# Kernel optimization log

Measured on AMD Instinct MI355X. Metric: run time of the kernel, lower is better.

The kernel has to match this reference:

```python
import jax, jax.numpy as jnp
import numpy as np

B, S, D = 4, 4096, 1024

def setup_inputs() -> dict:
    key = jax.random.key(0)
    k1, k2, k3 = jax.random.split(key, 3)
    x = jax.random.normal(k1, (B, S, D), dtype=jnp.float32)
    # learned scalar decay logit; original initializes to 0.9 then sigmoids it
    decay_param = jnp.float32(0.9)
    # gate weight [D, D]; original inits to zeros (identity module) -- use small
    # random values so the baseline exercises the full math path
    W_gate = jax.random.normal(k3, (D, D), dtype=jnp.float32) * 0.02
    return {"x": x, "decay_param": decay_param, "W_gate": W_gate}

def reference(x, decay_param, W_gate):
    # x: [B, S, D]
    d = jax.nn.sigmoid(decay_param)  # scalar

    def step(state, x_t):
        # state, x_t: [B, D]
        new = d * state + (1.0 - d) * x_t
        return new, new

    x_t_first = jnp.swapaxes(x, 0, 1)  # [S, B, D]
    init = jnp.zeros((x.shape[0], x.shape[2]), dtype=x.dtype)
    _, causal = jax.lax.scan(step, init, x_t_first)  # [S, B, D]
    causal = jnp.swapaxes(causal, 0, 1)  # [B, S, D]
    # nn.Linear(D, D, bias=False): y = causal @ W^T
    return x + jnp.einsum('bsd,ed->bse', causal, W_gate)
```

## Files before the change

### kernel.cpp

```cpp
#include <hip/hip_runtime.h>
#include <hip/hip_bf16.h>

#define B_DIM 4
#define S_DIM 4096
#define D_DIM 1024
#define M_TOT (B_DIM * S_DIM)
#define LOOKBACK 64
#define CHUNK 128
#define NT (D_DIM / 64)

typedef unsigned short us;
typedef __attribute__((ext_vector_type(8))) short bf16x8;
typedef __attribute__((ext_vector_type(4))) float f32x4;
typedef __attribute__((ext_vector_type(4))) unsigned short u16x4;

__device__ __forceinline__ us f2bf(float f) {
  unsigned int u = __builtin_bit_cast(unsigned int, f);
  u += 0x7fffu + ((u >> 16) & 1u);
  return (us)(u >> 16);
}

__global__ __launch_bounds__(256) void scan_kernel(
    const float* __restrict__ x, const float* __restrict__ dp,
    us* __restrict__ causal) {
  const float dcy = 1.0f / (1.0f + expf(-dp[0]));
  const float omd = 1.0f - dcy;
  const int d0 = blockIdx.x * 512 + threadIdx.x;
  const int s0 = blockIdx.y * CHUNK;
  const size_t base = (size_t)blockIdx.z * S_DIM * D_DIM + d0;
  float st0 = 0.f, st1 = 0.f;
  if (s0 > 0) {
    const float* px = x + base + (size_t)(s0 - LOOKBACK) * D_DIM;
#pragma unroll 8
    for (int i = 0; i < LOOKBACK; ++i) {
      st0 = dcy * st0 + omd * px[0];
      st1 = dcy * st1 + omd * px[256];
      px += D_DIM;
    }
  }
  const float* px = x + base + (size_t)s0 * D_DIM;
  us* pc = causal + base + (size_t)s0 * D_DIM;
#pragma unroll 8
  for (int i = 0; i < CHUNK; ++i) {
    st0 = dcy * st0 + omd * px[0];
    st1 = dcy * st1 + omd * px[256];
    pc[0]   = f2bf(st0);
    pc[256] = f2bf(st1);
    px += D_DIM;
    pc += D_DIM;
  }
}

__global__ __launch_bounds__(256) void convw_kernel(
    const float* __restrict__ W, us* __restrict__ Wb) {
  const int i = (blockIdx.x * 256 + threadIdx.x) * 4;
  const float4 v = *(const float4*)(W + i);
  u16x4 o;
  o.x = f2bf(v.x); o.y = f2bf(v.y); o.z = f2bf(v.z); o.w = f2bf(v.w);
  *(u16x4*)(Wb + i) = o;
}

__global__ __launch_bounds__(256) void gemm_kernel(
    const us* __restrict__ A,
    const us* __restrict__ Bw,
    const float* __restrict__ x,
    float* __restrict__ out) {
  __shared__ us As[128 * 64];
  __shared__ us Bs[128 * 64];

  const int bid = blockIdx.x;
  const int swz = (bid & 7) * 128 + (bid >> 3);
  const int m0 = (swz >> 3) * 128;
  const int n0 = (swz & 7) * 128;

  const int tid = threadIdx.x;
  const int lane = tid & 63;
  const int wave = tid >> 6;
  const int wr = wave >> 1;
  const int wc = wave & 1;
  const int lrow = lane & 15;
  const int ls   = lane >> 4;
  const int koff0 = ((0 + ls) ^ (lane & 7)) * 8;
  const int koff1 = ((4 + ls) ^ (lane & 7)) * 8;
  const int arow = (wr * 64 + lrow) * 64;
  const int brow = (wc * 64 + lrow) * 64;

  f32x4 acc[4][4];
#pragma unroll
  for (int i = 0; i < 4; ++i)
#pragma unroll
    for (int j = 0; j < 4; ++j) acc[i][j] = (f32x4)0.f;

  for (int t = 0; t < NT; ++t) {
    const int k0 = t * 64;
#pragma unroll
    for (int it = 0; it < 4; ++it) {
      const int c = it * 256 + tid;
      const int r = c >> 3;
      const int c16 = (c & 7) ^ (r & 7);
      __builtin_amdgcn_global_load_lds(
          (const __attribute__((address_space(1))) void*)(A +
              (size_t)(m0 + r) * D_DIM + k0 + c16 * 8),
          (__attribute__((address_space(3))) void*)(As + c * 8), 16, 0, 0);
      __builtin_amdgcn_global_load_lds(
          (const __attribute__((address_space(1))) void*)(Bw +
              (size_t)(n0 + r) * D_DIM + k0 + c16 * 8),
          (__attribute__((address_space(3))) void*)(Bs + c * 8), 16, 0, 0);
    }
    __syncthreads();

    bf16x8 a[4][2], b[4][2];
#pragma unroll
    for (int mi = 0; mi < 4; ++mi) {
      a[mi][0] = *(const bf16x8*)(As + arow + mi * 16 * 64 + koff0);
      a[mi][1] = *(const bf16x8*)(As + arow + mi * 16 * 64 + koff1);
    }
#pragma unroll
    for (int nj = 0; nj < 4; ++nj) {
      b[nj][0] = *(const bf16x8*)(Bs + brow + nj * 16 * 64 + koff0);
      b[nj][1] = *(const bf16x8*)(Bs + brow + nj * 16 * 64 + koff1);
    }
#pragma unroll
    for (int ks = 0; ks < 2; ++ks)
#pragma unroll
      for (int mi = 0; mi < 4; ++mi)
#pragma unroll
        for (int nj = 0; nj < 4; ++nj)
          acc[mi][nj] = __builtin_amdgcn_mfma_f32_16x16x32_bf16(
              a[mi][ks], b[nj][ks], acc[mi][nj], 0, 0, 0);
    __syncthreads();
  }

#pragma unroll
  for (int mi = 0; mi < 4; ++mi)
#pragma unroll
    for (int nj = 0; nj < 4; ++nj) {
      const int ocol = n0 + wc * 64 + nj * 16 + lrow;
      const int orow0 = m0 + wr * 64 + mi * 16 + ls * 4;
#pragma unroll
      for (int r = 0; r < 4; ++r) {
        const size_t idx = (size_t)(orow0 + r) * D_DIM + ocol;
        out[idx] = x[idx] + acc[mi][nj][r];
      }
    }
}

extern "C" void kernel_launch(void* const* d_in, const int* in_sizes, int n_in,
                              void* d_out, int out_size, void* d_ws, size_t ws_size,
                              hipStream_t stream) {
  const float* x  = (const float*)d_in[0];
  const float* dp = (const float*)d_in[1];
  const float* W  = (const float*)d_in[2];
  float* out = (float*)d_out;

  us* causal = (us*)d_ws;
  us* Wb = (us*)((char*)d_ws + (size_t)M_TOT * D_DIM * 2);

  dim3 g_scan(D_DIM / 512, S_DIM / CHUNK, B_DIM);
  scan_kernel<<<g_scan, 256, 0, stream>>>(x, dp, causal);

  convw_kernel<<<(D_DIM * D_DIM) / (256 * 4), 256, 0, stream>>>(W, Wb);

  gemm_kernel<<<(M_TOT / 128) * (D_DIM / 128), 256, 0, stream>>>(
      causal, Wb, x, out);
}
```

Measured before the change: 80.39 us.

## Double-buffer LDS in GEMM, shrink N tile to 64, remap block swizzle

The GEMM now double-buffers its A and B shared-memory tiles, issuing the async global-to-LDS loads for the next K step while the current step's MFMAs run, with one barrier per iteration. The output tile shrinks from 128x128 to 128x64, which doubles the grid, and the block-index swizzle is remapped. A launch-bounds occupancy hint of 3 blocks per CU is added. The intent is to hide global load latency and raise occupancy, at the cost of less operand reuse per block and more total A-tile traffic.

```diff
diff --git a/kernel.cpp b/kernel.cpp
--- a/kernel.cpp
+++ b/kernel.cpp
@@ -60,18 +60,18 @@
   *(u16x4*)(Wb + i) = o;
 }
 
-__global__ __launch_bounds__(256) void gemm_kernel(
+__global__ __launch_bounds__(256, 3) void gemm_kernel(
     const us* __restrict__ A,
     const us* __restrict__ Bw,
     const float* __restrict__ x,
     float* __restrict__ out) {
-  __shared__ us As[128 * 64];
-  __shared__ us Bs[128 * 64];
+  __shared__ us As[2][128 * 64];
+  __shared__ us Bs[2][64 * 64];
 
   const int bid = blockIdx.x;
-  const int swz = (bid & 7) * 128 + (bid >> 3);
-  const int m0 = (swz >> 3) * 128;
-  const int n0 = (swz & 7) * 128;
+  const int q = bid >> 3;
+  const int m0 = (((bid & 7) << 4) + (q >> 4)) * 128;
+  const int n0 = (q & 15) * 64;
 
   const int tid = threadIdx.x;
   const int lane = tid & 63;
@@ -83,59 +83,72 @@
   const int koff0 = ((0 + ls) ^ (lane & 7)) * 8;
   const int koff1 = ((4 + ls) ^ (lane & 7)) * 8;
   const int arow = (wr * 64 + lrow) * 64;
-  const int brow = (wc * 64 + lrow) * 64;
+  const int brow = (wc * 32 + lrow) * 64;
 
-  f32x4 acc[4][4];
+  f32x4 acc[4][2];
 #pragma unroll
   for (int i = 0; i < 4; ++i)
 #pragma unroll
-    for (int j = 0; j < 4; ++j) acc[i][j] = (f32x4)0.f;
+    for (int j = 0; j < 2; ++j) acc[i][j] = (f32x4)0.f;
+
+#define STAGE(t, p)                                                            \
+  {                                                                            \
+    _Pragma("unroll")                                                          \
+    for (int it = 0; it < 4; ++it) {                                           \
+      const int c = it * 256 + tid;                                            \
+      const int r = c >> 3;                                                    \
+      const int slot = (c & 7) ^ (r & 7);                                      \
+      __builtin_amdgcn_global_load_lds(                                        \
+          (const __attribute__((address_space(1))) void*)(A +                  \
+              (size_t)(m0 + r) * D_DIM + (t) * 64 + slot * 8),                 \
+          (__attribute__((address_space(3))) void*)(&As[p][0] + c * 8),        \
+          16, 0, 0);                                                           \
+    }                                                                          \
+    _Pragma("unroll")                                                          \
+    for (int it = 0; it < 2; ++it) {                                           \
+      const int c = it * 256 + tid;                                            \
+      const int r = c >> 3;                                                    \
+      const int slot = (c & 7) ^ (r & 7);                                      \
+      __builtin_amdgcn_global_load_lds(                                        \
+          (const __attribute__((address_space(1))) void*)(Bw +                 \
+              (size_t)(n0 + r) * D_DIM + (t) * 64 + slot * 8),                 \
+          (__attribute__((address_space(3))) void*)(&Bs[p][0] + c * 8),        \
+          16, 0, 0);                                                           \
+    }                                                                          \
+  }
+
+  STAGE(0, 0);
+  __syncthreads();
 
   for (int t = 0; t < NT; ++t) {
-    const int k0 = t * 64;
+    const int p = t & 1;
+    if (t + 1 < NT) STAGE(t + 1, p ^ 1);
+
 #pragma unroll
-    for (int it = 0; it < 4; ++it) {
-      const int c = it * 256 + tid;
-      const int r = c >> 3;
-      const int c16 = (c & 7) ^ (r & 7);
-      __builtin_amdgcn_global_load_lds(
-          (const __attribute__((address_space(1))) void*)(A +
-              (size_t)(m0 + r) * D_DIM + k0 + c16 * 8),
-          (__attribute__((address_space(3))) void*)(As + c * 8), 16, 0, 0);
-      __builtin_amdgcn_global_load_lds(
-          (const __attribute__((address_space(1))) void*)(Bw +
-              (size_t)(n0 + r) * D_DIM + k0 + c16 * 8),
-          (__attribute__((address_space(3))) void*)(Bs + c * 8), 16, 0, 0);
-    }
-    __syncthreads();
-
-    bf16x8 a[4][2], b[4][2];
+    for (int ks = 0; ks < 2; ++ks) {
+      const int koff = ks ? koff1 : koff0;
+      bf16x8 a[4], b[2];
 #pragma unroll
-    for (int mi = 0; mi < 4; ++mi) {
-      a[mi][0] = *(const bf16x8*)(As + arow + mi * 16 * 64 + koff0);
-      a[mi][1] = *(const bf16x8*)(As + arow + mi * 16 * 64 + koff1);
-    }
+      for (int mi = 0; mi < 4; ++mi)
+        a[mi] = *(const bf16x8*)(&As[p][0] + arow + mi * 1024 + koff);
 #pragma unroll
-    for (int nj = 0; nj < 4; ++nj) {
-      b[nj][0] = *(const bf16x8*)(Bs + brow + nj * 16 * 64 + koff0);
-      b[nj][1] = *(const bf16x8*)(Bs + brow + nj * 16 * 64 + koff1);
-    }
-#pragma unroll
-    for (int ks = 0; ks < 2; ++ks)
+      for (int nj = 0; nj < 2; ++nj)
+        b[nj] = *(const bf16x8*)(&Bs[p][0] + brow + nj * 1024 + koff);
 #pragma unroll
       for (int mi = 0; mi < 4; ++mi)
 #pragma unroll
-        for (int nj = 0; nj < 4; ++nj)
+        for (int nj = 0; nj < 2; ++nj)
           acc[mi][nj] = __builtin_amdgcn_mfma_f32_16x16x32_bf16(
-              a[mi][ks], b[nj][ks], acc[mi][nj], 0, 0, 0);
+              a[mi], b[nj], acc[mi][nj], 0, 0, 0);
+    }
     __syncthreads();
   }
 
 #pragma unroll
   for (int mi = 0; mi < 4; ++mi)
 #pragma unroll
-    for (int nj = 0; nj < 4; ++nj) {
-      const int ocol = n0 + wc * 64 + nj * 16 + lrow;
+    for (int nj = 0; nj < 2; ++nj) {
+      const int ocol = n0 + wc * 32 + nj * 16 + lrow;
       const int orow0 = m0 + wr * 64 + mi * 16 + ls * 4;
 #pragma unroll
       for (int r = 0; r < 4; ++r) {
@@ -143,6 +156,7 @@
         out[idx] = x[idx] + acc[mi][nj][r];
       }
     }
+#undef STAGE
 }
 
 extern "C" void kernel_launch(void* const* d_in, const int* in_sizes, int n_in,
@@ -161,6 +175,6 @@
 
   convw_kernel<<<(D_DIM * D_DIM) / (256 * 4), 256, 0, stream>>>(W, Wb);
 
-  gemm_kernel<<<(M_TOT / 128) * (D_DIM / 128), 256, 0, stream>>>(
+  gemm_kernel<<<(M_TOT / 128) * (D_DIM / 64), 256, 0, stream>>>(
       causal, Wb, x, out);
 }
```

After: 82.68 us. 2.9% more time.

## Double-buffer GEMM LDS tiles with interleaved prefetch and MFMA quarters

Applied to the files above, without the earlier changes.

Restructures the GEMM main loop into a double-buffered LDS pipeline. The A tile is prefetched two steps ahead and the B tile one step ahead, with loads split into halves and interleaved between quarter-blocks of MFMAs. Explicit vmcnt waits, raw s_barrier and setprio around MFMAs replace the full __syncthreads pairs. It also changes the XCD-aware block-to-tile mapping and requests two blocks per CU. This is meant to hide global-to-LDS latency behind compute. In exchange it uses 64KB of LDS and relies on hand-tuned waitcnt correctness.

```diff
diff --git a/kernel.cpp b/kernel.cpp
--- a/kernel.cpp
+++ b/kernel.cpp
@@ -60,18 +60,18 @@
   *(u16x4*)(Wb + i) = o;
 }
 
-__global__ __launch_bounds__(256) void gemm_kernel(
+__global__ __launch_bounds__(256, 2) void gemm_kernel(
     const us* __restrict__ A,
     const us* __restrict__ Bw,
     const float* __restrict__ x,
     float* __restrict__ out) {
-  __shared__ us As[128 * 64];
-  __shared__ us Bs[128 * 64];
+  __shared__ us smem_s[32768];
 
   const int bid = blockIdx.x;
-  const int swz = (bid & 7) * 128 + (bid >> 3);
-  const int m0 = (swz >> 3) * 128;
-  const int n0 = (swz & 7) * 128;
+  const int xcd = bid & 7;
+  const int q = bid >> 3;
+  const int m0 = (xcd * 16 + (q >> 3)) * 128;
+  const int n0 = (q & 7) * 128;
 
   const int tid = threadIdx.x;
   const int lane = tid & 63;
@@ -91,44 +91,92 @@
 #pragma unroll
     for (int j = 0; j < 4; ++j) acc[i][j] = (f32x4)0.f;
 
+#define STAGE_HALF(SRC, rowbase, t, h, ldsdst)                                 \
+  {                                                                            \
+    _Pragma("unroll")                                                          \
+    for (int it = 0; it < 2; ++it) {                                           \
+      const int c = it * 256 + tid;                                \
+      const int r = c >> 3;                                        \
+      const int slot = (c & 7) ^ (r & 7);                                      \
+      __builtin_amdgcn_global_load_lds(                                        \
+          (const __attribute__((address_space(1))) void*)((SRC) +              \
+              (size_t)((rowbase) + (h) * 64 + r) * D_DIM + (t) * 64 + slot * 8),\
+          (__attribute__((address_space(3))) void*)((ldsdst) + (h) * 4096 + c * 8),\
+          16, 0, 0);                                                           \
+    }                                                                          \
+  }
+#define BAR() __builtin_amdgcn_s_barrier()
+#define MFMA_Q(MI0, NJ0)                                                       \
+  __builtin_amdgcn_s_setprio(1);                                               \
+  _Pragma("unroll")                                                            \
+  for (int ks = 0; ks < 2; ++ks)                                               \
+    _Pragma("unroll")                                                          \
+    for (int mi = 0; mi < 2; ++mi)                                             \
+      _Pragma("unroll")                                                        \
+      for (int nj = 0; nj < 2; ++nj)                                           \
+        acc[(MI0) + mi][(NJ0) + nj] = __builtin_amdgcn_mfma_f32_16x16x32_bf16( \
+            a[(MI0) + mi][ks], b[(NJ0) + nj][ks], acc[(MI0) + mi][(NJ0) + nj], \
+            0, 0, 0);                                                          \
+  __builtin_amdgcn_s_setprio(0)
+
+  us* const A0b = smem_s;
+  us* const B0b = smem_s + 8192;
+  us* const A1b = smem_s + 16384;
+
+  STAGE_HALF(A,  m0, 0, 0, A0b); STAGE_HALF(A,  m0, 0, 1, A0b);
+  STAGE_HALF(Bw, n0, 0, 0, B0b); STAGE_HALF(Bw, n0, 0, 1, B0b);
+  STAGE_HALF(A,  m0, 1, 0, A1b); STAGE_HALF(A,  m0, 1, 1, A1b);
+  asm volatile("s_waitcnt vmcnt(4)" ::: "memory");
+  BAR();
+
+  bf16x8 a[4][2], b[4][2];
+
   for (int t = 0; t < NT; ++t) {
-    const int k0 = t * 64;
-#pragma unroll
-    for (int it = 0; it < 4; ++it) {
-      const int c = it * 256 + tid;
-      const int r = c >> 3;
-      const int c16 = (c & 7) ^ (r & 7);
-      __builtin_amdgcn_global_load_lds(
-          (const __attribute__((address_space(1))) void*)(A +
-              (size_t)(m0 + r) * D_DIM + k0 + c16 * 8),
-          (__attribute__((address_space(3))) void*)(As + c * 8), 16, 0, 0);
-      __builtin_amdgcn_global_load_lds(
-          (const __attribute__((address_space(1))) void*)(Bw +
-              (size_t)(n0 + r) * D_DIM + k0 + c16 * 8),
-          (__attribute__((address_space(3))) void*)(Bs + c * 8), 16, 0, 0);
-    }
-    __syncthreads();
-
-    bf16x8 a[4][2], b[4][2];
-#pragma unroll
-    for (int mi = 0; mi < 4; ++mi) {
-      a[mi][0] = *(const bf16x8*)(As + arow + mi * 16 * 64 + koff0);
-      a[mi][1] = *(const bf16x8*)(As + arow + mi * 16 * 64 + koff1);
-    }
-#pragma unroll
-    for (int nj = 0; nj < 4; ++nj) {
-      b[nj][0] = *(const bf16x8*)(Bs + brow + nj * 16 * 64 + koff0);
-      b[nj][1] = *(const bf16x8*)(Bs + brow + nj * 16 * 64 + koff1);
-    }
-#pragma unroll
-    for (int ks = 0; ks < 2; ++ks)
-#pragma unroll
-      for (int mi = 0; mi < 4; ++mi)
-#pragma unroll
-        for (int nj = 0; nj < 4; ++nj)
-          acc[mi][nj] = __builtin_amdgcn_mfma_f32_16x16x32_bf16(
-              a[mi][ks], b[nj][ks], acc[mi][nj], 0, 0, 0);
-    __syncthreads();
+    const int p = t & 1;
+    us* const Ab  = smem_s + p * 16384;
+    us* const Bb  = Ab + 8192;
+    us* const Bbn = smem_s + (p ^ 1) * 16384 + 8192;
+
+#pragma unroll
+    for (int mi = 0; mi < 2; ++mi) {
+      a[mi][0] = *(const bf16x8*)(Ab + arow + mi * 1024 + koff0);
+      a[mi][1] = *(const bf16x8*)(Ab + arow + mi * 1024 + koff1);
+    }
+#pragma unroll
+    for (int nj = 0; nj < 2; ++nj) {
+      b[nj][0] = *(const bf16x8*)(Bb + brow + nj * 1024 + koff0);
+      b[nj][1] = *(const bf16x8*)(Bb + brow + nj * 1024 + koff1);
+    }
+    if (t + 1 < NT) STAGE_HALF(Bw, n0, t + 1, 0, Bbn);
+    BAR();
+    MFMA_Q(0, 0);
+
+#pragma unroll
+    for (int mi = 2; mi < 4; ++mi) {
+      a[mi][0] = *(const bf16x8*)(Ab + arow + mi * 1024 + koff0);
+      a[mi][1] = *(const bf16x8*)(Ab + arow + mi * 1024 + koff1);
+    }
+    if (t + 1 < NT) STAGE_HALF(Bw, n0, t + 1, 1, Bbn);
+    BAR();
+    MFMA_Q(2, 0);
+
+#pragma unroll
+    for (int nj = 2; nj < 4; ++nj) {
+      b[nj][0] = *(const bf16x8*)(Bb + brow + nj * 1024 + koff0);
+      b[nj][1] = *(const bf16x8*)(Bb + brow + nj * 1024 + koff1);
+    }
+    if (t + 2 < NT) STAGE_HALF(A, m0, t + 2, 0, Ab);
+    BAR();
+    MFMA_Q(0, 2);
+
+    if (t + 2 < NT) STAGE_HALF(A, m0, t + 2, 1, Ab);
+    if (t + 2 < NT) {
+      asm volatile("s_waitcnt vmcnt(4)" ::: "memory");
+    } else if (t + 1 < NT) {
+      asm volatile("s_waitcnt vmcnt(0)" ::: "memory");
+    }
+    BAR();
+    MFMA_Q(2, 2);
   }
 
 #pragma unroll
@@ -143,6 +191,9 @@
         out[idx] = x[idx] + acc[mi][nj][r];
       }
     }
+#undef STAGE_HALF
+#undef BAR
+#undef MFMA_Q
 }
 
 extern "C" void kernel_launch(void* const* d_in, const int* in_sizes, int n_in,
```

After: 71.93 us. 1.12x faster.
